# Kernel optimization log

Measured on AMD Instinct MI355X. Metric: run time of the kernel, lower is better.

## Reference

```python
import jax, jax.numpy as jnp
import numpy as np

B, T, E, HID, V, K = 32, 512, 512, 512, 50257, 12
H = HID // 2          # per-direction LSTM hidden
START, STOP = 10, 11  # tag_to_ix['<START>'], tag_to_ix['<STOP>']
NEG = -10000.0


def setup_inputs() -> dict:
    key = jax.random.key(0)
    ks = jax.random.split(key, 16)
    sentence = jax.random.randint(ks[0], (B, T), 0, V)
    embed = jax.random.normal(ks[1], (V, E), jnp.float32) * 0.1
    # torch LSTM weights, gate order (i, f, g, o); biases fused (b_ih + b_hh)
    w_ih_f = jax.random.normal(ks[2], (4 * H, E), jnp.float32) * 0.05
    w_hh_f = jax.random.normal(ks[3], (4 * H, H), jnp.float32) * 0.05
    b_f = jax.random.normal(ks[4], (4 * H,), jnp.float32) * 0.05
    w_ih_b = jax.random.normal(ks[5], (4 * H, E), jnp.float32) * 0.05
    w_hh_b = jax.random.normal(ks[6], (4 * H, H), jnp.float32) * 0.05
    b_b = jax.random.normal(ks[7], (4 * H,), jnp.float32) * 0.05
    # init_hidden(): random initial states, [2 directions, B, H]
    h0 = jax.random.normal(ks[8], (2, B, H), jnp.float32)
    c0 = jax.random.normal(ks[9], (2, B, H), jnp.float32)
    W_out = jax.random.normal(ks[10], (K, HID), jnp.float32) * 0.05
    b_out = jax.random.normal(ks[11], (K,), jnp.float32) * 0.05
    transitions = jax.random.normal(ks[12], (K, K), jnp.float32)
    transitions = transitions.at[START, :].set(NEG).at[:, STOP].set(NEG)
    return dict(sentence=sentence, embed=embed,
                w_ih_f=w_ih_f, w_hh_f=w_hh_f, b_f=b_f,
                w_ih_b=w_ih_b, w_hh_b=w_hh_b, b_b=b_b,
                h0=h0, c0=c0, W_out=W_out, b_out=b_out,
                transitions=transitions)


def _lstm_dir(x, w_ih, w_hh, b, h0, c0, reverse):
    # x: [B, T, E] -> hidden sequence [B, T, H]
    xg = jnp.einsum('bte,ge->btg', x, w_ih) + b  # [B, T, 4H] input pre-activations

    def step(carry, xt):
        h, c = carry
        g = xt + h @ w_hh.T
        i, f, gg, o = jnp.split(g, 4, axis=-1)
        c = jax.nn.sigmoid(f) * c + jax.nn.sigmoid(i) * jnp.tanh(gg)
        h = jax.nn.sigmoid(o) * jnp.tanh(c)
        return (h, c), h

    _, ys = jax.lax.scan(step, (h0, c0), jnp.swapaxes(xg, 0, 1), reverse=reverse)
    return jnp.swapaxes(ys, 0, 1)


def reference(sentence, embed, w_ih_f, w_hh_f, b_f, w_ih_b, w_hh_b, b_b,
              h0, c0, W_out, b_out, transitions):
    # _get_lstm_features
    x = embed[sentence]  # [B, T, E]
    hf = _lstm_dir(x, w_ih_f, w_hh_f, b_f, h0[0], c0[0], False)
    hb = _lstm_dir(x, w_ih_b, w_hh_b, b_b, h0[1], c0[1], True)
    feats = jnp.concatenate([hf, hb], axis=-1) @ W_out.T + b_out  # [B, T, K]

    # _viterbi_decode: fused per-timestep max/argmax recurrence
    init = jnp.full((B, K), NEG, jnp.float32).at[:, START].set(0.0)

    def vstep(fv, feat_t):
        # scores[b, next, prev] = fv[b, prev] + transitions[next, prev]
        scores = fv[:, None, :] + transitions[None, :, :]
        bptr = jnp.argmax(scores, axis=2)            # [B, K]
        fv_new = jnp.max(scores, axis=2) + feat_t     # emit score added after max
        return fv_new, bptr

    fv, bptrs = jax.lax.scan(vstep, init, jnp.swapaxes(feats, 0, 1))  # bptrs [T, B, K]
    terminal = fv + transitions[STOP]                 # [B, K]
    best = jnp.argmax(terminal, axis=1)               # [B]
    # faithful to original: terminal_var[:, best_tag_id] -> [B, B]
    path_score = jnp.take(terminal, best, axis=1)

    def back(tag, bp):
        prev = jnp.take_along_axis(bp, tag[:, None], axis=1)[:, 0]
        return prev, prev

    _, ys = jax.lax.scan(back, best, bptrs, reverse=True)  # ys[t] = tag at position t-1
    # path positions 0..T-1 are (ys[1:], best); ys[0] is START (dropped by [:,1:])
    best_path = jnp.concatenate([ys[1:], best[None, :]], axis=0).T  # [B, T]
    return path_score, best_path
```

## Files before the change

### kernel.cpp

```cpp
#include <hip/hip_runtime.h>
#include <hip/hip_bf16.h>


typedef __attribute__((ext_vector_type(8))) __bf16 bf16x8;
typedef __attribute__((ext_vector_type(8))) unsigned short u16x8;
typedef __attribute__((ext_vector_type(4))) float  f32x4;

#define MFMA16(a, b, c) __builtin_amdgcn_mfma_f32_16x16x32_bf16((a), (b), (c), 0, 0, 0)

__device__ __forceinline__ float sigm(float x) { return 1.0f / (1.0f + __expf(-x)); }
__device__ __forceinline__ float tanh_f(float x) {
  x = fminf(fmaxf(x, -15.0f), 15.0f);
  float e = __expf(2.0f * x);
  return (e - 1.0f) / (e + 1.0f);
}

__device__ __forceinline__ void split8(const float* v, bf16x8& hi, bf16x8& lo) {
#pragma unroll
  for (int j = 0; j < 8; j++) {
    __bf16 h = (__bf16)v[j];
    hi[j] = h;
    lo[j] = (__bf16)(v[j] - (float)h);
  }
}

__global__ __launch_bounds__(256) void xg_gemm(
    const int* __restrict__ sent, const float* __restrict__ embed,
    const float* __restrict__ wih_f, const float* __restrict__ wih_b,
    const float* __restrict__ bias_f, const float* __restrict__ bias_b,
    float* __restrict__ xg)
{
  __shared__ __bf16 Ah[128][40], Al[128][40];
  __shared__ __bf16 Bh[128][40], Bl[128][40];
  __shared__ int toks[128];
  const int tid = threadIdx.x;
  const int m0 = blockIdx.x * 128, n0 = blockIdx.y * 128;
  if (tid < 128) toks[tid] = sent[m0 + tid];
  const int wave = tid >> 6, lane = tid & 63, q = lane >> 4, c = lane & 15;
  const int wy = wave >> 1, wx = wave & 1;
  f32x4 acc[4][4];
  for (int mt = 0; mt < 4; mt++)
    for (int nt = 0; nt < 4; nt++)
      acc[mt][nt] = f32x4{0.0f, 0.0f, 0.0f, 0.0f};
  __syncthreads();

  for (int k0 = 0; k0 < 512; k0 += 32) {
#pragma unroll
    for (int i = 0; i < 2; i++) {
      int ch = tid + (i << 8);
      int r = ch >> 2, kc = ch & 3;
      float tmp[8];
      const float* asrc = embed + (size_t)toks[r] * 512 + k0 + kc * 8;
#pragma unroll
      for (int j = 0; j < 8; j++) tmp[j] = asrc[j];
      bf16x8 hi, lo;
      split8(tmp, hi, lo);
      *(bf16x8*)&Ah[r][kc * 8] = hi;
      *(bf16x8*)&Al[r][kc * 8] = lo;
      int n = n0 + r;
      const float* wsrc = (n < 1024) ? (wih_f + (size_t)n * 512)
                                     : (wih_b + (size_t)(n - 1024) * 512);
#pragma unroll
      for (int j = 0; j < 8; j++) tmp[j] = wsrc[k0 + kc * 8 + j];
      split8(tmp, hi, lo);
      *(bf16x8*)&Bh[r][kc * 8] = hi;
      *(bf16x8*)&Bl[r][kc * 8] = lo;
    }
    __syncthreads();
    bf16x8 ah[4], al[4], bh[4], bl[4];
#pragma unroll
    for (int t4 = 0; t4 < 4; t4++) {
      int ar = wy * 64 + t4 * 16 + c, br = wx * 64 + t4 * 16 + c;
      ah[t4] = *(const bf16x8*)&Ah[ar][q * 8];
      al[t4] = *(const bf16x8*)&Al[ar][q * 8];
      bh[t4] = *(const bf16x8*)&Bh[br][q * 8];
      bl[t4] = *(const bf16x8*)&Bl[br][q * 8];
    }
#pragma unroll
    for (int mt = 0; mt < 4; mt++)
#pragma unroll
      for (int nt = 0; nt < 4; nt++) {
        acc[mt][nt] = MFMA16(ah[mt], bh[nt], acc[mt][nt]);
        acc[mt][nt] = MFMA16(al[mt], bh[nt], acc[mt][nt]);
        acc[mt][nt] = MFMA16(ah[mt], bl[nt], acc[mt][nt]);
      }
    __syncthreads();
  }

#pragma unroll
  for (int nt = 0; nt < 4; nt++) {
    int n = n0 + wx * 64 + nt * 16 + c;
    float bval = (n < 1024) ? bias_f[n] : bias_b[n - 1024];
#pragma unroll
    for (int mt = 0; mt < 4; mt++) {
      int mbase = m0 + wy * 64 + mt * 16 + q * 4;
#pragma unroll
      for (int reg = 0; reg < 4; reg++)
        xg[(size_t)(mbase + reg) * 2048 + n] = acc[mt][nt][reg] + bval;
    }
  }
}

__global__ __launch_bounds__(256, 1) void lstm_rec(
    const float* __restrict__ xg,
    const float* __restrict__ whh_f, const float* __restrict__ whh_b,
    const float* __restrict__ h0, const float* __restrict__ c0,
    float* __restrict__ h_seq,
    unsigned int* __restrict__ hx,
    int* __restrict__ flags)
{
  const int blk = blockIdx.x;
  const int d = blk >> 2, hs = blk & 3;
  const int tid = threadIdx.x;
  const int wave = tid >> 6, lane = tid & 63, q = lane >> 4, c = lane & 15;
  const float* __restrict__ whh = d ? whh_b : whh_f;

  __shared__ __bf16 hfrag[2][16][512];

  bf16x8 wfh[4][8], wfl[4][8];
#pragma unroll
  for (int g = 0; g < 4; g++) {
    int row = g * 256 + hs * 64 + wave * 16 + c;
    const float* wr = whh + (size_t)row * 256;
#pragma unroll
    for (int ks = 0; ks < 8; ks++) {
      float tmp[8];
#pragma unroll
      for (int j = 0; j < 8; j++) tmp[j] = wr[ks * 32 + q * 8 + j];
      split8(tmp, wfh[g][ks], wfl[g][ks]);
    }
  }
  const int ug = hs * 64 + wave * 16 + c;
  float cst[2][4];
#pragma unroll
  for (int mt = 0; mt < 2; mt++)
#pragma unroll
    for (int reg = 0; reg < 4; reg++)
      cst[mt][reg] = c0[d * 8192 + (mt * 16 + q * 4 + reg) * 256 + ug];

  const int sb = tid >> 3;
  const int kc4 = (tid & 7) * 4;

  for (int s = 0; s < 512; s++) {
    const int t_seq = d ? (511 - s) : s;
    const int p = s & 1;

    float xv[2][4][4];
#pragma unroll
    for (int mt = 0; mt < 2; mt++)
#pragma unroll
      for (int reg = 0; reg < 4; reg++) {
        int b = mt * 16 + q * 4 + reg;
        const float* xr = xg + ((size_t)(b * 512 + t_seq) << 11) + (d << 10) + ug;
#pragma unroll
        for (int g = 0; g < 4; g++)
          xv[mt][g][reg] = xr[g << 8];
      }

    if (s > 0) {
      if (tid == 0) {
        while (__hip_atomic_load(&flags[d * 512 + s - 1], __ATOMIC_RELAXED,
                                 __HIP_MEMORY_SCOPE_AGENT) < 4)
          __builtin_amdgcn_s_sleep(1);
      }
      __syncthreads();
    }

    if (s == 0) {
#pragma unroll
      for (int i = 0; i < 4; i++) {
        int kc = kc4 + i;
        float tmp[8];
        const float* src = h0 + d * 8192 + sb * 256 + kc * 8;
#pragma unroll
        for (int j = 0; j < 8; j++) tmp[j] = src[j];
        bf16x8 vhi, vlo;
        split8(tmp, vhi, vlo);
        int fid = ((sb >> 4) << 3) + (kc >> 2);
        int cid = ((kc & 3) << 4) + (sb & 15);
        int pos = cid ^ (fid & 7);
        *(bf16x8*)&hfrag[0][fid][pos * 8] = vhi;
        *(bf16x8*)&hfrag[1][fid][pos * 8] = vlo;
      }
    } else {
      unsigned int vals[4][8];
      const unsigned int* hb = hx + ((size_t)((d * 2 + p) * 32 + sb)) * 256 + kc4 * 8;
#pragma unroll
      for (int i = 0; i < 4; i++)
#pragma unroll
        for (int j = 0; j < 8; j++)
          vals[i][j] = __hip_atomic_load(hb + i * 8 + j, __ATOMIC_RELAXED,
                                         __HIP_MEMORY_SCOPE_AGENT);
#pragma unroll
      for (int i = 0; i < 4; i++) {
        int kc = kc4 + i;
        u16x8 vhi, vlo;
#pragma unroll
        for (int j = 0; j < 8; j++) {
          vhi[j] = (unsigned short)(vals[i][j] >> 16);
          vlo[j] = (unsigned short)(vals[i][j] & 0xffffu);
        }
        int fid = ((sb >> 4) << 3) + (kc >> 2);
        int cid = ((kc & 3) << 4) + (sb & 15);
        int pos = cid ^ (fid & 7);
        *(u16x8*)&hfrag[0][fid][pos * 8] = vhi;
        *(u16x8*)&hfrag[1][fid][pos * 8] = vlo;
      }
    }

    f32x4 acc[2][4];
#pragma unroll
    for (int mt = 0; mt < 2; mt++)
#pragma unroll
      for (int g = 0; g < 4; g++)
#pragma unroll
        for (int reg = 0; reg < 4; reg++)
          acc[mt][g][reg] = xv[mt][g][reg];

    __syncthreads();

#pragma unroll
    for (int ks = 0; ks < 8; ks++) {
      int pos = (lane ^ ks) * 8;
      bf16x8 ahi0 = *(const bf16x8*)&hfrag[0][ks][pos];
      bf16x8 ahi1 = *(const bf16x8*)&hfrag[0][8 + ks][pos];
      bf16x8 alo0 = *(const bf16x8*)&hfrag[1][ks][pos];
      bf16x8 alo1 = *(const bf16x8*)&hfrag[1][8 + ks][pos];
#pragma unroll
      for (int g = 0; g < 4; g++) {
        acc[0][g] = MFMA16(ahi0, wfh[g][ks], acc[0][g]);
        acc[1][g] = MFMA16(ahi1, wfh[g][ks], acc[1][g]);
        acc[0][g] = MFMA16(alo0, wfh[g][ks], acc[0][g]);
        acc[1][g] = MFMA16(alo1, wfh[g][ks], acc[1][g]);
        acc[0][g] = MFMA16(ahi0, wfl[g][ks], acc[0][g]);
        acc[1][g] = MFMA16(ahi1, wfl[g][ks], acc[1][g]);
      }
    }

    const int pn = (s + 1) & 1;
#pragma unroll
    for (int mt = 0; mt < 2; mt++)
#pragma unroll
      for (int reg = 0; reg < 4; reg++) {
        int b = mt * 16 + q * 4 + reg;
        float iv = sigm(acc[mt][0][reg]);
        float fg = sigm(acc[mt][1][reg]);
        float gv = tanh_f(acc[mt][2][reg]);
        float ov = sigm(acc[mt][3][reg]);
        float cn = fg * cst[mt][reg] + iv * gv;
        cst[mt][reg] = cn;
        float hn = ov * tanh_f(cn);
        h_seq[((size_t)(b * 512 + t_seq) << 9) + (d << 8) + ug] = hn;
        __bf16 hhi = (__bf16)hn;
        __bf16 hlo = (__bf16)(hn - (float)hhi);
        unsigned int pack =
            ((unsigned int)__builtin_bit_cast(unsigned short, hhi) << 16) |
            (unsigned int)__builtin_bit_cast(unsigned short, hlo);
        __hip_atomic_store(&hx[((size_t)((d * 2 + pn) * 32 + b)) * 256 + ug], pack,
                           __ATOMIC_RELAXED, __HIP_MEMORY_SCOPE_AGENT);
      }

    __syncthreads();
    if (tid == 0)
      __hip_atomic_fetch_add(&flags[d * 512 + s], 1, __ATOMIC_RELAXED,
                             __HIP_MEMORY_SCOPE_AGENT);
  }
}

__global__ __launch_bounds__(256) void feats_k(
    const float* __restrict__ h_seq, const float* __restrict__ W_out,
    const float* __restrict__ b_out, float* __restrict__ feats)
{
  int m = blockIdx.x * 4 + (threadIdx.x >> 6);
  int lane = threadIdx.x & 63;
  const float4* hp = (const float4*)(h_seq + (size_t)m * 512 + lane * 8);
  float4 a = hp[0], b2 = hp[1];
  float h[8] = {a.x, a.y, a.z, a.w, b2.x, b2.y, b2.z, b2.w};
#pragma unroll
  for (int k = 0; k < 12; k++) {
    const float4* wp = (const float4*)(W_out + k * 512 + lane * 8);
    float4 w0 = wp[0], w1 = wp[1];
    float w[8] = {w0.x, w0.y, w0.z, w0.w, w1.x, w1.y, w1.z, w1.w};
    float p = 0.0f;
#pragma unroll
    for (int j = 0; j < 8; j++) p += h[j] * w[j];
#pragma unroll
    for (int off = 32; off > 0; off >>= 1) p += __shfl_xor(p, off);
    if (lane == 0) feats[(size_t)m * 12 + k] = p + b_out[k];
  }
}

__global__ __launch_bounds__(64) void viterbi_k(
    const float* __restrict__ feats, const float* __restrict__ trans,
    float* __restrict__ terminal, int* __restrict__ best,
    float* __restrict__ out_path)
{
  const int b = blockIdx.x;
  const int lane = threadIdx.x;
  __shared__ unsigned char bp[512][12];
  float trow[12];
#pragma unroll
  for (int pv = 0; pv < 12; pv++)
    trow[pv] = (lane < 12) ? trans[lane * 12 + pv] : -10000.0f;
  float fv = (lane == 10) ? 0.0f : -10000.0f;
  for (int t = 0; t < 512; t++) {
    float bestv = -3.4e38f;
    int arg = 0;
#pragma unroll
    for (int pv = 0; pv < 12; pv++) {
      float sc = __shfl(fv, pv) + trow[pv];
      if (sc > bestv) { bestv = sc; arg = pv; }
    }
    float ft = (lane < 12) ? feats[(size_t)(b * 512 + t) * 12 + lane] : 0.0f;
    if (lane < 12) {
      bp[t][lane] = (unsigned char)arg;
      fv = bestv + ft;
    }
  }
  float term = fv + ((lane < 12) ? trans[11 * 12 + lane] : 0.0f);
  if (lane < 12) terminal[b * 12 + lane] = term;
  float v = (lane < 12) ? term : -3.4e38f;
  int idx = lane;
#pragma unroll
  for (int off = 8; off > 0; off >>= 1) {
    float ov = __shfl_down(v, off);
    int oi = __shfl_down(idx, off);
    if (ov > v || (ov == v && oi < idx)) { v = ov; idx = oi; }
  }
  int bidx = __shfl(idx, 0);
  __syncthreads();
  if (lane == 0) {
    best[b] = bidx;
    int tag = bidx;
    out_path[b * 512 + 511] = (float)bidx;
    for (int t = 511; t >= 1; t--) {
      tag = bp[t][tag];
      out_path[b * 512 + t - 1] = (float)tag;
    }
  }
}

__global__ __launch_bounds__(256) void pscore_k(
    const float* __restrict__ terminal, const int* __restrict__ best,
    float* __restrict__ out)
{
  int idx = blockIdx.x * 256 + threadIdx.x;
  if (idx < 1024) {
    int i = idx >> 5, j = idx & 31;
    out[idx] = terminal[i * 12 + best[j]];
  }
}

extern "C" void kernel_launch(void* const* d_in, const int* in_sizes, int n_in,
                              void* d_out, int out_size, void* d_ws, size_t ws_size,
                              hipStream_t stream)
{
  const int*   sent  = (const int*)d_in[0];
  const float* embed = (const float*)d_in[1];
  const float* wih_f = (const float*)d_in[2];
  const float* whh_f = (const float*)d_in[3];
  const float* b_f   = (const float*)d_in[4];
  const float* wih_b = (const float*)d_in[5];
  const float* whh_b = (const float*)d_in[6];
  const float* b_b   = (const float*)d_in[7];
  const float* h0    = (const float*)d_in[8];
  const float* c0    = (const float*)d_in[9];
  const float* W_out = (const float*)d_in[10];
  const float* b_out = (const float*)d_in[11];
  const float* trans = (const float*)d_in[12];

  char* ws = (char*)d_ws;
  float*        xg    = (float*)(ws);
  float*        h_seq = (float*)(ws + 134217728);
  float*        feats = (float*)(ws + 167772160);
  unsigned int* hx    = (unsigned int*)(ws + 168558592);
  int*          flags = (int*)(ws + 168689664);
  float*        term  = (float*)(ws + 168693760);
  int*          best  = (int*)(ws + 168695296);

  float* outp = (float*)d_out;

  hipMemsetAsync(flags, 0, 2 * 512 * sizeof(int), stream);
  xg_gemm<<<dim3(128, 16), 256, 0, stream>>>(sent, embed, wih_f, wih_b, b_f, b_b, xg);
  lstm_rec<<<8, 256, 0, stream>>>(xg, whh_f, whh_b, h0, c0, h_seq, hx, flags);
  feats_k<<<4096, 256, 0, stream>>>(h_seq, W_out, b_out, feats);
  viterbi_k<<<32, 64, 0, stream>>>(feats, trans, term, best, outp + 1024);
  pscore_k<<<4, 256, 0, stream>>>(term, best, outp);
}
```

Before: 4.594 ms.

## Replace per-step flag barrier with step-tagged hidden-state words in LSTM recurrence

The cross-block handshake in the recurrent LSTM kernel no longer uses a separate flag counter. Each hidden value is now stored as a 64-bit word that carries the step number in its upper half. Readers spin directly on the data until every word they need shows the expected tag. This removes the end-of-step barrier, the flag atomic and the separate flag poll from the serial 512-step critical path. To keep the removed barrier safe, the LDS hidden fragment is double-buffered by step parity. In exchange, the exchanged hidden buffer doubles in width, each reader polls many words instead of one flag, and the buffer now aliases the feats region of the workspace.

```diff
diff --git a/kernel.cpp b/kernel.cpp
--- a/kernel.cpp
+++ b/kernel.cpp
@@ -106,8 +106,7 @@
     const float* __restrict__ whh_f, const float* __restrict__ whh_b,
     const float* __restrict__ h0, const float* __restrict__ c0,
     float* __restrict__ h_seq,
-    unsigned int* __restrict__ hx,
-    int* __restrict__ flags)
+    unsigned long long* __restrict__ hx)
 {
   const int blk = blockIdx.x;
   const int d = blk >> 2, hs = blk & 3;
@@ -115,7 +114,7 @@
   const int wave = tid >> 6, lane = tid & 63, q = lane >> 4, c = lane & 15;
   const float* __restrict__ whh = d ? whh_b : whh_f;
 
-  __shared__ __bf16 hfrag[2][16][512];
+  __shared__ __bf16 hfrag[2][2][16][512];
 
   bf16x8 wfh[4][8], wfl[4][8];
 #pragma unroll
@@ -156,15 +155,6 @@
         for (int g = 0; g < 4; g++)
           xv[mt][g][reg] = xr[g << 8];
       }
-
-    if (s > 0) {
-      if (tid == 0) {
-        while (__hip_atomic_load(&flags[d * 512 + s - 1], __ATOMIC_RELAXED,
-                                 __HIP_MEMORY_SCOPE_AGENT) < 4)
-          __builtin_amdgcn_s_sleep(1);
-      }
-      __syncthreads();
-    }
 
     if (s == 0) {
 #pragma unroll
@@ -179,32 +169,52 @@
         int fid = ((sb >> 4) << 3) + (kc >> 2);
         int cid = ((kc & 3) << 4) + (sb & 15);
         int pos = cid ^ (fid & 7);
-        *(bf16x8*)&hfrag[0][fid][pos * 8] = vhi;
-        *(bf16x8*)&hfrag[1][fid][pos * 8] = vlo;
+        *(bf16x8*)&hfrag[0][0][fid][pos * 8] = vhi;
+        *(bf16x8*)&hfrag[0][1][fid][pos * 8] = vlo;
       }
     } else {
-      unsigned int vals[4][8];
-      const unsigned int* hb = hx + ((size_t)((d * 2 + p) * 32 + sb)) * 256 + kc4 * 8;
+      const unsigned long long want = (unsigned long long)s;
+      unsigned long long v[4][8];
+      const unsigned long long* hb =
+          hx + ((size_t)((d * 2 + p) * 32 + sb)) * 256 + kc4 * 8;
 #pragma unroll
       for (int i = 0; i < 4; i++)
 #pragma unroll
         for (int j = 0; j < 8; j++)
-          vals[i][j] = __hip_atomic_load(hb + i * 8 + j, __ATOMIC_RELAXED,
-                                         __HIP_MEMORY_SCOPE_AGENT);
+          v[i][j] = __hip_atomic_load(hb + i * 8 + j, __ATOMIC_RELAXED,
+                                      __HIP_MEMORY_SCOPE_AGENT);
+      while (true) {
+        bool ok = true;
+#pragma unroll
+        for (int i = 0; i < 4; i++)
+#pragma unroll
+          for (int j = 0; j < 8; j++)
+            if ((v[i][j] >> 32) != want) ok = false;
+        if (ok) break;
+        __builtin_amdgcn_s_sleep(1);
+#pragma unroll
+        for (int i = 0; i < 4; i++)
+#pragma unroll
+          for (int j = 0; j < 8; j++)
+            if ((v[i][j] >> 32) != want)
+              v[i][j] = __hip_atomic_load(hb + i * 8 + j, __ATOMIC_RELAXED,
+                                          __HIP_MEMORY_SCOPE_AGENT);
+      }
 #pragma unroll
       for (int i = 0; i < 4; i++) {
         int kc = kc4 + i;
         u16x8 vhi, vlo;
 #pragma unroll
         for (int j = 0; j < 8; j++) {
-          vhi[j] = (unsigned short)(vals[i][j] >> 16);
-          vlo[j] = (unsigned short)(vals[i][j] & 0xffffu);
+          unsigned int pack = (unsigned int)v[i][j];
+          vhi[j] = (unsigned short)(pack >> 16);
+          vlo[j] = (unsigned short)(pack & 0xffffu);
         }
         int fid = ((sb >> 4) << 3) + (kc >> 2);
         int cid = ((kc & 3) << 4) + (sb & 15);
         int pos = cid ^ (fid & 7);
-        *(u16x8*)&hfrag[0][fid][pos * 8] = vhi;
-        *(u16x8*)&hfrag[1][fid][pos * 8] = vlo;
+        *(u16x8*)&hfrag[p][0][fid][pos * 8] = vhi;
+        *(u16x8*)&hfrag[p][1][fid][pos * 8] = vlo;
       }
     }
 
@@ -222,10 +232,10 @@
 #pragma unroll
     for (int ks = 0; ks < 8; ks++) {
       int pos = (lane ^ ks) * 8;
-      bf16x8 ahi0 = *(const bf16x8*)&hfrag[0][ks][pos];
-      bf16x8 ahi1 = *(const bf16x8*)&hfrag[0][8 + ks][pos];
-      bf16x8 alo0 = *(const bf16x8*)&hfrag[1][ks][pos];
-      bf16x8 alo1 = *(const bf16x8*)&hfrag[1][8 + ks][pos];
+      bf16x8 ahi0 = *(const bf16x8*)&hfrag[p][0][ks][pos];
+      bf16x8 ahi1 = *(const bf16x8*)&hfrag[p][0][8 + ks][pos];
+      bf16x8 alo0 = *(const bf16x8*)&hfrag[p][1][ks][pos];
+      bf16x8 alo1 = *(const bf16x8*)&hfrag[p][1][8 + ks][pos];
 #pragma unroll
       for (int g = 0; g < 4; g++) {
         acc[0][g] = MFMA16(ahi0, wfh[g][ks], acc[0][g]);
@@ -238,6 +248,7 @@
     }
 
     const int pn = (s + 1) & 1;
+    const unsigned long long tag = ((unsigned long long)(s + 1)) << 32;
 #pragma unroll
     for (int mt = 0; mt < 2; mt++)
 #pragma unroll
@@ -256,14 +267,10 @@
         unsigned int pack =
             ((unsigned int)__builtin_bit_cast(unsigned short, hhi) << 16) |
             (unsigned int)__builtin_bit_cast(unsigned short, hlo);
-        __hip_atomic_store(&hx[((size_t)((d * 2 + pn) * 32 + b)) * 256 + ug], pack,
+        __hip_atomic_store(&hx[((size_t)((d * 2 + pn) * 32 + b)) * 256 + ug],
+                           tag | (unsigned long long)pack,
                            __ATOMIC_RELAXED, __HIP_MEMORY_SCOPE_AGENT);
       }
-
-    __syncthreads();
-    if (tid == 0)
-      __hip_atomic_fetch_add(&flags[d * 512 + s], 1, __ATOMIC_RELAXED,
-                             __HIP_MEMORY_SCOPE_AGENT);
   }
 }
 
@@ -370,19 +377,18 @@
   const float* trans = (const float*)d_in[12];
 
   char* ws = (char*)d_ws;
-  float*        xg    = (float*)(ws);
-  float*        h_seq = (float*)(ws + 134217728);
-  float*        feats = (float*)(ws + 167772160);
-  unsigned int* hx    = (unsigned int*)(ws + 168558592);
-  int*          flags = (int*)(ws + 168689664);
-  float*        term  = (float*)(ws + 168693760);
-  int*          best  = (int*)(ws + 168695296);
+  float*              xg    = (float*)(ws);
+  float*              h_seq = (float*)(ws + 134217728);
+  float*              feats = (float*)(ws + 167772160);
+  unsigned long long* hx    = (unsigned long long*)(ws + 167772160);
+  float*              term  = (float*)(ws + 168558592);
+  int*                best  = (int*)(ws + 168560128);
 
   float* outp = (float*)d_out;
 
-  hipMemsetAsync(flags, 0, 2 * 512 * sizeof(int), stream);
+  hipMemsetAsync(hx, 0, 2 * 2 * 32 * 256 * sizeof(unsigned long long), stream);
   xg_gemm<<<dim3(128, 16), 256, 0, stream>>>(sent, embed, wih_f, wih_b, b_f, b_b, xg);
-  lstm_rec<<<8, 256, 0, stream>>>(xg, whh_f, whh_b, h0, c0, h_seq, hx, flags);
+  lstm_rec<<<8, 256, 0, stream>>>(xg, whh_f, whh_b, h0, c0, h_seq, hx);
   feats_k<<<4096, 256, 0, stream>>>(h_seq, W_out, b_out, feats);
   viterbi_k<<<32, 64, 0, stream>>>(feats, trans, term, best, outp + 1024);
   pscore_k<<<4, 256, 0, stream>>>(term, best, outp);
```

New measurement: 5.089 ms. +10.8%, slower.

## Use per-wave flag signaling and double-buffered LDS in LSTM recurrence

Applied to the files above, without the earlier changes.

Drops the block-wide barrier and single-thread spin in the persistent LSTM recurrence. Each wave now polls the step flag itself (waiting for 16 wave arrivals) and signals with its own lane-0 atomic once its hx stores drain. The hidden-state LDS buffer is double-buffered by step parity, which removes the trailing __syncthreads. The hx exchange uses 64-bit atomic loads, and the h_seq store plus the next step's xg prefetch are moved off the critical path after the signal. The cost is more atomic traffic on the flag counters and more registers for the prefetched inputs, and it relies on vmcnt(0) ordering for correctness.

```diff
diff --git a/kernel.cpp b/kernel.cpp
--- a/kernel.cpp
+++ b/kernel.cpp
@@ -115,7 +115,7 @@
   const int wave = tid >> 6, lane = tid & 63, q = lane >> 4, c = lane & 15;
   const float* __restrict__ whh = d ? whh_b : whh_f;
 
-  __shared__ __bf16 hfrag[2][16][512];
+  __shared__ __bf16 hfrag[2][2][16][512];
 
   bf16x8 wfh[4][8], wfl[4][8];
 #pragma unroll
@@ -141,30 +141,25 @@
   const int sb = tid >> 3;
   const int kc4 = (tid & 7) * 4;
 
+  auto load_xv = [&](float (&xv)[2][4][4], int tt) {
+#pragma unroll
+    for (int mt = 0; mt < 2; mt++)
+#pragma unroll
+      for (int reg = 0; reg < 4; reg++) {
+        int b = mt * 16 + q * 4 + reg;
+        const float* xr = xg + ((size_t)(b * 512 + tt) << 11) + (d << 10) + ug;
+#pragma unroll
+        for (int g = 0; g < 4; g++)
+          xv[mt][g][reg] = xr[g << 8];
+      }
+  };
+
+  float xv_cur[2][4][4];
+  load_xv(xv_cur, d ? 511 : 0);
+
   for (int s = 0; s < 512; s++) {
     const int t_seq = d ? (511 - s) : s;
     const int p = s & 1;
-
-    float xv[2][4][4];
-#pragma unroll
-    for (int mt = 0; mt < 2; mt++)
-#pragma unroll
-      for (int reg = 0; reg < 4; reg++) {
-        int b = mt * 16 + q * 4 + reg;
-        const float* xr = xg + ((size_t)(b * 512 + t_seq) << 11) + (d << 10) + ug;
-#pragma unroll
-        for (int g = 0; g < 4; g++)
-          xv[mt][g][reg] = xr[g << 8];
-      }
-
-    if (s > 0) {
-      if (tid == 0) {
-        while (__hip_atomic_load(&flags[d * 512 + s - 1], __ATOMIC_RELAXED,
-                                 __HIP_MEMORY_SCOPE_AGENT) < 4)
-          __builtin_amdgcn_s_sleep(1);
-      }
-      __syncthreads();
-    }
 
     if (s == 0) {
 #pragma unroll
@@ -179,32 +174,38 @@
         int fid = ((sb >> 4) << 3) + (kc >> 2);
         int cid = ((kc & 3) << 4) + (sb & 15);
         int pos = cid ^ (fid & 7);
-        *(bf16x8*)&hfrag[0][fid][pos * 8] = vhi;
-        *(bf16x8*)&hfrag[1][fid][pos * 8] = vlo;
+        *(bf16x8*)&hfrag[0][0][fid][pos * 8] = vhi;
+        *(bf16x8*)&hfrag[0][1][fid][pos * 8] = vlo;
       }
     } else {
-      unsigned int vals[4][8];
-      const unsigned int* hb = hx + ((size_t)((d * 2 + p) * 32 + sb)) * 256 + kc4 * 8;
-#pragma unroll
-      for (int i = 0; i < 4; i++)
-#pragma unroll
-        for (int j = 0; j < 8; j++)
-          vals[i][j] = __hip_atomic_load(hb + i * 8 + j, __ATOMIC_RELAXED,
-                                         __HIP_MEMORY_SCOPE_AGENT);
+      while (__hip_atomic_load(&flags[d * 512 + s - 1], __ATOMIC_RELAXED,
+                               __HIP_MEMORY_SCOPE_AGENT) < 16)
+        __builtin_amdgcn_s_sleep(1);
+
+      const unsigned long long* hb64 = (const unsigned long long*)
+          (hx + ((size_t)((d * 2 + p) * 32 + sb)) * 256 + kc4 * 8);
+      unsigned long long v64[16];
+#pragma unroll
+      for (int i = 0; i < 16; i++)
+        v64[i] = __hip_atomic_load(hb64 + i, __ATOMIC_RELAXED,
+                                   __HIP_MEMORY_SCOPE_AGENT);
 #pragma unroll
       for (int i = 0; i < 4; i++) {
         int kc = kc4 + i;
         u16x8 vhi, vlo;
 #pragma unroll
         for (int j = 0; j < 8; j++) {
-          vhi[j] = (unsigned short)(vals[i][j] >> 16);
-          vlo[j] = (unsigned short)(vals[i][j] & 0xffffu);
+          unsigned long long dv = v64[i * 4 + (j >> 1)];
+          unsigned int w32 = (j & 1) ? (unsigned int)(dv >> 32)
+                                     : (unsigned int)dv;
+          vhi[j] = (unsigned short)(w32 >> 16);
+          vlo[j] = (unsigned short)(w32 & 0xffffu);
         }
         int fid = ((sb >> 4) << 3) + (kc >> 2);
         int cid = ((kc & 3) << 4) + (sb & 15);
         int pos = cid ^ (fid & 7);
-        *(u16x8*)&hfrag[0][fid][pos * 8] = vhi;
-        *(u16x8*)&hfrag[1][fid][pos * 8] = vlo;
+        *(u16x8*)&hfrag[p][0][fid][pos * 8] = vhi;
+        *(u16x8*)&hfrag[p][1][fid][pos * 8] = vlo;
       }
     }
 
@@ -215,17 +216,17 @@
       for (int g = 0; g < 4; g++)
 #pragma unroll
         for (int reg = 0; reg < 4; reg++)
-          acc[mt][g][reg] = xv[mt][g][reg];
+          acc[mt][g][reg] = xv_cur[mt][g][reg];
 
     __syncthreads();
 
 #pragma unroll
     for (int ks = 0; ks < 8; ks++) {
       int pos = (lane ^ ks) * 8;
-      bf16x8 ahi0 = *(const bf16x8*)&hfrag[0][ks][pos];
-      bf16x8 ahi1 = *(const bf16x8*)&hfrag[0][8 + ks][pos];
-      bf16x8 alo0 = *(const bf16x8*)&hfrag[1][ks][pos];
-      bf16x8 alo1 = *(const bf16x8*)&hfrag[1][8 + ks][pos];
+      bf16x8 ahi0 = *(const bf16x8*)&hfrag[p][0][ks][pos];
+      bf16x8 ahi1 = *(const bf16x8*)&hfrag[p][0][8 + ks][pos];
+      bf16x8 alo0 = *(const bf16x8*)&hfrag[p][1][ks][pos];
+      bf16x8 alo1 = *(const bf16x8*)&hfrag[p][1][8 + ks][pos];
 #pragma unroll
       for (int g = 0; g < 4; g++) {
         acc[0][g] = MFMA16(ahi0, wfh[g][ks], acc[0][g]);
@@ -238,6 +239,7 @@
     }
 
     const int pn = (s + 1) & 1;
+    float hv[2][4];
 #pragma unroll
     for (int mt = 0; mt < 2; mt++)
 #pragma unroll
@@ -250,7 +252,7 @@
         float cn = fg * cst[mt][reg] + iv * gv;
         cst[mt][reg] = cn;
         float hn = ov * tanh_f(cn);
-        h_seq[((size_t)(b * 512 + t_seq) << 9) + (d << 8) + ug] = hn;
+        hv[mt][reg] = hn;
         __bf16 hhi = (__bf16)hn;
         __bf16 hlo = (__bf16)(hn - (float)hhi);
         unsigned int pack =
@@ -260,10 +262,30 @@
                            __ATOMIC_RELAXED, __HIP_MEMORY_SCOPE_AGENT);
       }
 
-    __syncthreads();
-    if (tid == 0)
+    asm volatile("s_waitcnt vmcnt(0)" ::: "memory");
+    if (lane == 0)
       __hip_atomic_fetch_add(&flags[d * 512 + s], 1, __ATOMIC_RELAXED,
                              __HIP_MEMORY_SCOPE_AGENT);
+
+#pragma unroll
+    for (int mt = 0; mt < 2; mt++)
+#pragma unroll
+      for (int reg = 0; reg < 4; reg++) {
+        int b = mt * 16 + q * 4 + reg;
+        h_seq[((size_t)(b * 512 + t_seq) << 9) + (d << 8) + ug] = hv[mt][reg];
+      }
+
+    if (s < 511) {
+      float xv_nxt[2][4][4];
+      load_xv(xv_nxt, d ? (511 - (s + 1)) : (s + 1));
+#pragma unroll
+      for (int mt = 0; mt < 2; mt++)
+#pragma unroll
+        for (int g = 0; g < 4; g++)
+#pragma unroll
+          for (int reg = 0; reg < 4; reg++)
+            xv_cur[mt][g][reg] = xv_nxt[mt][g][reg];
+    }
   }
 }
 
```

New measurement: 4.002 ms. 1.15x faster.

## Replace block-barrier flag counting with per-wave flags and prefetch next-step inputs

Applied to the files above, without the earlier changes.

The recurrent LSTM kernel now has each wave publish its own per-step flag slot, and all lanes of every wave poll the 16 producer flags with a wave-wide vote. This replaces the single-thread spin, the block barrier and the atomic counter increment. The xg input for the next step is prefetched into alternating register buffers, and the shared h fragment buffer is double-buffered, which drops one __syncthreads per step. The hi/lo unpacking uses 64-bit loads and byte-permute instructions, and the h_seq store is moved after the flag publish. In exchange, the flags array grows 16x, register pressure rises, and correctness now rests on the explicit vmcnt wait ordering the hx stores before the flag store.

```diff
diff --git a/kernel.cpp b/kernel.cpp
--- a/kernel.cpp
+++ b/kernel.cpp
@@ -3,8 +3,8 @@
 
 
 typedef __attribute__((ext_vector_type(8))) __bf16 bf16x8;
-typedef __attribute__((ext_vector_type(8))) unsigned short u16x8;
 typedef __attribute__((ext_vector_type(4))) float  f32x4;
+typedef __attribute__((ext_vector_type(4))) unsigned int u32x4;
 
 #define MFMA16(a, b, c) __builtin_amdgcn_mfma_f32_16x16x32_bf16((a), (b), (c), 0, 0, 0)
 
@@ -115,7 +115,7 @@
   const int wave = tid >> 6, lane = tid & 63, q = lane >> 4, c = lane & 15;
   const float* __restrict__ whh = d ? whh_b : whh_f;
 
-  __shared__ __bf16 hfrag[2][16][512];
+  __shared__ __bf16 hfrag[2][2][16][512];
 
   bf16x8 wfh[4][8], wfl[4][8];
 #pragma unroll
@@ -141,130 +141,175 @@
   const int sb = tid >> 3;
   const int kc4 = (tid & 7) * 4;
 
-  for (int s = 0; s < 512; s++) {
-    const int t_seq = d ? (511 - s) : s;
-    const int p = s & 1;
-
-    float xv[2][4][4];
-#pragma unroll
-    for (int mt = 0; mt < 2; mt++)
-#pragma unroll
-      for (int reg = 0; reg < 4; reg++) {
-        int b = mt * 16 + q * 4 + reg;
-        const float* xr = xg + ((size_t)(b * 512 + t_seq) << 11) + (d << 10) + ug;
-#pragma unroll
-        for (int g = 0; g < 4; g++)
-          xv[mt][g][reg] = xr[g << 8];
-      }
-
-    if (s > 0) {
-      if (tid == 0) {
-        while (__hip_atomic_load(&flags[d * 512 + s - 1], __ATOMIC_RELAXED,
-                                 __HIP_MEMORY_SCOPE_AGENT) < 4)
-          __builtin_amdgcn_s_sleep(1);
-      }
-      __syncthreads();
-    }
-
-    if (s == 0) {
-#pragma unroll
-      for (int i = 0; i < 4; i++) {
-        int kc = kc4 + i;
-        float tmp[8];
-        const float* src = h0 + d * 8192 + sb * 256 + kc * 8;
-#pragma unroll
-        for (int j = 0; j < 8; j++) tmp[j] = src[j];
-        bf16x8 vhi, vlo;
-        split8(tmp, vhi, vlo);
-        int fid = ((sb >> 4) << 3) + (kc >> 2);
-        int cid = ((kc & 3) << 4) + (sb & 15);
-        int pos = cid ^ (fid & 7);
-        *(bf16x8*)&hfrag[0][fid][pos * 8] = vhi;
-        *(bf16x8*)&hfrag[1][fid][pos * 8] = vlo;
-      }
-    } else {
-      unsigned int vals[4][8];
-      const unsigned int* hb = hx + ((size_t)((d * 2 + p) * 32 + sb)) * 256 + kc4 * 8;
-#pragma unroll
-      for (int i = 0; i < 4; i++)
-#pragma unroll
-        for (int j = 0; j < 8; j++)
-          vals[i][j] = __hip_atomic_load(hb + i * 8 + j, __ATOMIC_RELAXED,
-                                         __HIP_MEMORY_SCOPE_AGENT);
-#pragma unroll
-      for (int i = 0; i < 4; i++) {
-        int kc = kc4 + i;
-        u16x8 vhi, vlo;
-#pragma unroll
-        for (int j = 0; j < 8; j++) {
-          vhi[j] = (unsigned short)(vals[i][j] >> 16);
-          vlo[j] = (unsigned short)(vals[i][j] & 0xffffu);
-        }
-        int fid = ((sb >> 4) << 3) + (kc >> 2);
-        int cid = ((kc & 3) << 4) + (sb & 15);
-        int pos = cid ^ (fid & 7);
-        *(u16x8*)&hfrag[0][fid][pos * 8] = vhi;
-        *(u16x8*)&hfrag[1][fid][pos * 8] = vlo;
-      }
-    }
-
-    f32x4 acc[2][4];
-#pragma unroll
-    for (int mt = 0; mt < 2; mt++)
+  int fid_c[4], pos_c[4];
+#pragma unroll
+  for (int i = 0; i < 4; i++) {
+    int kc = kc4 + i;
+    fid_c[i] = ((sb >> 4) << 3) + (kc >> 2);
+    pos_c[i] = ((((kc & 3) << 4) + (sb & 15)) ^ (fid_c[i] & 7));
+  }
+
+  const unsigned long long* hb64p[2];
+  hb64p[0] = (const unsigned long long*)(hx + ((size_t)((d * 2 + 0) * 32 + sb)) * 256 + kc4 * 8);
+  hb64p[1] = (const unsigned long long*)(hx + ((size_t)((d * 2 + 1) * 32 + sb)) * 256 + kc4 * 8);
+  const int hwbase0 = (d * 2 + 0) * 32 * 256 + ug;
+  const int hwbase1 = (d * 2 + 1) * 32 * 256 + ug;
+  int bof[2][4];
+#pragma unroll
+  for (int mt = 0; mt < 2; mt++)
+#pragma unroll
+    for (int reg = 0; reg < 4; reg++)
+      bof[mt][reg] = (mt * 16 + q * 4 + reg) * 256;
+
+  int fro = (d * 512) * 16 + (lane & 15);
+  int fwo = (d * 512) * 16 + hs * 4 + wave;
+
+  const int t0 = d ? 511 : 0;
+  const int tdelt = d ? -2048 : 2048;
+  const int sdelt = d ? -512 : 512;
+
+  int xgo[2][4], hso[2][4];
+#pragma unroll
+  for (int mt = 0; mt < 2; mt++)
+#pragma unroll
+    for (int reg = 0; reg < 4; reg++) {
+      int b = mt * 16 + q * 4 + reg;
+      xgo[mt][reg] = (b * 512 + t0) * 2048 + (d << 10) + ug;
+      hso[mt][reg] = (b * 512 + t0) * 512 + (d << 8) + ug;
+    }
+
+  float xvA[2][4][4], xvB[2][4][4];
+#pragma unroll
+  for (int mt = 0; mt < 2; mt++)
+#pragma unroll
+    for (int reg = 0; reg < 4; reg++)
 #pragma unroll
       for (int g = 0; g < 4; g++)
-#pragma unroll
-        for (int reg = 0; reg < 4; reg++)
-          acc[mt][g][reg] = xv[mt][g][reg];
-
-    __syncthreads();
-
-#pragma unroll
-    for (int ks = 0; ks < 8; ks++) {
-      int pos = (lane ^ ks) * 8;
-      bf16x8 ahi0 = *(const bf16x8*)&hfrag[0][ks][pos];
-      bf16x8 ahi1 = *(const bf16x8*)&hfrag[0][8 + ks][pos];
-      bf16x8 alo0 = *(const bf16x8*)&hfrag[1][ks][pos];
-      bf16x8 alo1 = *(const bf16x8*)&hfrag[1][8 + ks][pos];
-#pragma unroll
-      for (int g = 0; g < 4; g++) {
-        acc[0][g] = MFMA16(ahi0, wfh[g][ks], acc[0][g]);
-        acc[1][g] = MFMA16(ahi1, wfh[g][ks], acc[1][g]);
-        acc[0][g] = MFMA16(alo0, wfh[g][ks], acc[0][g]);
-        acc[1][g] = MFMA16(alo1, wfh[g][ks], acc[1][g]);
-        acc[0][g] = MFMA16(ahi0, wfl[g][ks], acc[0][g]);
-        acc[1][g] = MFMA16(ahi1, wfl[g][ks], acc[1][g]);
-      }
-    }
-
-    const int pn = (s + 1) & 1;
-#pragma unroll
-    for (int mt = 0; mt < 2; mt++)
-#pragma unroll
-      for (int reg = 0; reg < 4; reg++) {
-        int b = mt * 16 + q * 4 + reg;
-        float iv = sigm(acc[mt][0][reg]);
-        float fg = sigm(acc[mt][1][reg]);
-        float gv = tanh_f(acc[mt][2][reg]);
-        float ov = sigm(acc[mt][3][reg]);
-        float cn = fg * cst[mt][reg] + iv * gv;
-        cst[mt][reg] = cn;
-        float hn = ov * tanh_f(cn);
-        h_seq[((size_t)(b * 512 + t_seq) << 9) + (d << 8) + ug] = hn;
-        __bf16 hhi = (__bf16)hn;
-        __bf16 hlo = (__bf16)(hn - (float)hhi);
-        unsigned int pack =
-            ((unsigned int)__builtin_bit_cast(unsigned short, hhi) << 16) |
-            (unsigned int)__builtin_bit_cast(unsigned short, hlo);
-        __hip_atomic_store(&hx[((size_t)((d * 2 + pn) * 32 + b)) * 256 + ug], pack,
-                           __ATOMIC_RELAXED, __HIP_MEMORY_SCOPE_AGENT);
-      }
-
-    __syncthreads();
-    if (tid == 0)
-      __hip_atomic_fetch_add(&flags[d * 512 + s], 1, __ATOMIC_RELAXED,
-                             __HIP_MEMORY_SCOPE_AGENT);
-  }
+        xvA[mt][g][reg] = xg[xgo[mt][reg] + (g << 8)];
+
+#define LSTM_STEP(S_, P_, XC_, XN_)                                           \
+  {                                                                           \
+    if ((S_) == 0) {                                                          \
+      _Pragma("unroll")                                                       \
+      for (int i = 0; i < 4; i++) {                                           \
+        int kc = kc4 + i;                                                     \
+        float tmp[8];                                                         \
+        const float* src = h0 + d * 8192 + sb * 256 + kc * 8;                 \
+        _Pragma("unroll")                                                     \
+        for (int j = 0; j < 8; j++) tmp[j] = src[j];                          \
+        bf16x8 vhi, vlo;                                                      \
+        split8(tmp, vhi, vlo);                                                \
+        *(bf16x8*)&hfrag[0][0][fid_c[i]][pos_c[i] * 8] = vhi;                 \
+        *(bf16x8*)&hfrag[0][1][fid_c[i]][pos_c[i] * 8] = vlo;                 \
+      }                                                                       \
+    } else {                                                                  \
+      int fv = __hip_atomic_load(flags + fro, __ATOMIC_RELAXED,               \
+                                 __HIP_MEMORY_SCOPE_AGENT);                   \
+      while (!__all(fv == (S_))) {                                            \
+        __builtin_amdgcn_s_sleep(1);                                          \
+        fv = __hip_atomic_load(flags + fro, __ATOMIC_RELAXED,                 \
+                               __HIP_MEMORY_SCOPE_AGENT);                     \
+      }                                                                       \
+      fro += 16;                                                              \
+      unsigned long long v64[16];                                             \
+      _Pragma("unroll")                                                       \
+      for (int i = 0; i < 16; i++)                                            \
+        v64[i] = __hip_atomic_load(hb64p[P_] + i, __ATOMIC_RELAXED,           \
+                                   __HIP_MEMORY_SCOPE_AGENT);                 \
+      _Pragma("unroll")                                                       \
+      for (int i = 0; i < 4; i++) {                                           \
+        u32x4 vh, vl;                                                         \
+        _Pragma("unroll")                                                     \
+        for (int k = 0; k < 4; k++) {                                         \
+          unsigned int lo32 = (unsigned int)v64[i * 4 + k];                   \
+          unsigned int hi32 = (unsigned int)(v64[i * 4 + k] >> 32);           \
+          vh[k] = __builtin_amdgcn_perm(hi32, lo32, 0x07060302u);             \
+          vl[k] = __builtin_amdgcn_perm(hi32, lo32, 0x05040100u);             \
+        }                                                                     \
+        *(u32x4*)&hfrag[P_][0][fid_c[i]][pos_c[i] * 8] = vh;                  \
+        *(u32x4*)&hfrag[P_][1][fid_c[i]][pos_c[i] * 8] = vl;                  \
+      }                                                                       \
+    }                                                                         \
+    f32x4 acc[2][4];                                                          \
+    _Pragma("unroll")                                                         \
+    for (int mt = 0; mt < 2; mt++)                                            \
+      _Pragma("unroll")                                                       \
+      for (int g = 0; g < 4; g++)                                             \
+        _Pragma("unroll")                                                     \
+        for (int reg = 0; reg < 4; reg++)                                     \
+          acc[mt][g][reg] = XC_[mt][g][reg];                                  \
+    __syncthreads();                                                          \
+    _Pragma("unroll")                                                         \
+    for (int ks = 0; ks < 8; ks++) {                                          \
+      int pos = (lane ^ ks) * 8;                                              \
+      bf16x8 ahi0 = *(const bf16x8*)&hfrag[P_][0][ks][pos];                   \
+      bf16x8 ahi1 = *(const bf16x8*)&hfrag[P_][0][8 + ks][pos];               \
+      bf16x8 alo0 = *(const bf16x8*)&hfrag[P_][1][ks][pos];                   \
+      bf16x8 alo1 = *(const bf16x8*)&hfrag[P_][1][8 + ks][pos];               \
+      _Pragma("unroll")                                                       \
+      for (int g = 0; g < 4; g++) {                                           \
+        acc[0][g] = MFMA16(ahi0, wfh[g][ks], acc[0][g]);                      \
+        acc[1][g] = MFMA16(ahi1, wfh[g][ks], acc[1][g]);                      \
+        acc[0][g] = MFMA16(alo0, wfh[g][ks], acc[0][g]);                      \
+        acc[1][g] = MFMA16(alo1, wfh[g][ks], acc[1][g]);                      \
+        acc[0][g] = MFMA16(ahi0, wfl[g][ks], acc[0][g]);                      \
+        acc[1][g] = MFMA16(ahi1, wfl[g][ks], acc[1][g]);                      \
+      }                                                                       \
+    }                                                                         \
+    float hv[2][4];                                                           \
+    _Pragma("unroll")                                                         \
+    for (int mt = 0; mt < 2; mt++)                                            \
+      _Pragma("unroll")                                                       \
+      for (int reg = 0; reg < 4; reg++) {                                     \
+        float iv = sigm(acc[mt][0][reg]);                                     \
+        float fg = sigm(acc[mt][1][reg]);                                     \
+        float gv = tanh_f(acc[mt][2][reg]);                                   \
+        float ov = sigm(acc[mt][3][reg]);                                     \
+        float cn = fg * cst[mt][reg] + iv * gv;                               \
+        cst[mt][reg] = cn;                                                    \
+        float hn = ov * tanh_f(cn);                                           \
+        hv[mt][reg] = hn;                                                     \
+        __bf16 hhi = (__bf16)hn;                                              \
+        __bf16 hlo = (__bf16)(hn - (float)hhi);                               \
+        unsigned int pack =                                                   \
+            ((unsigned int)__builtin_bit_cast(unsigned short, hhi) << 16) |   \
+            (unsigned int)__builtin_bit_cast(unsigned short, hlo);            \
+        __hip_atomic_store(hx + ((P_) ? hwbase0 : hwbase1) + bof[mt][reg],    \
+                           pack, __ATOMIC_RELAXED, __HIP_MEMORY_SCOPE_AGENT); \
+      }                                                                       \
+    asm volatile("s_waitcnt vmcnt(0)" ::: "memory");                          \
+    if (lane == 0)                                                            \
+      __hip_atomic_store(flags + fwo, (S_) + 1, __ATOMIC_RELAXED,             \
+                         __HIP_MEMORY_SCOPE_AGENT);                           \
+    fwo += 16;                                                                \
+    _Pragma("unroll")                                                         \
+    for (int mt = 0; mt < 2; mt++)                                            \
+      _Pragma("unroll")                                                       \
+      for (int reg = 0; reg < 4; reg++)                                       \
+        h_seq[hso[mt][reg]] = hv[mt][reg];                                    \
+    if ((S_) < 511) {                                                         \
+      _Pragma("unroll")                                                       \
+      for (int mt = 0; mt < 2; mt++)                                          \
+        _Pragma("unroll")                                                     \
+        for (int reg = 0; reg < 4; reg++) {                                   \
+          xgo[mt][reg] += tdelt;                                              \
+          hso[mt][reg] += sdelt;                                              \
+        }                                                                     \
+      _Pragma("unroll")                                                       \
+      for (int mt = 0; mt < 2; mt++)                                          \
+        _Pragma("unroll")                                                     \
+        for (int reg = 0; reg < 4; reg++)                                     \
+          _Pragma("unroll")                                                   \
+          for (int g = 0; g < 4; g++)                                         \
+            XN_[mt][g][reg] = xg[xgo[mt][reg] + (g << 8)];                    \
+    }                                                                         \
+  }
+
+  for (int s = 0; s < 512; s += 2) {
+    LSTM_STEP(s,     0, xvA, xvB);
+    LSTM_STEP(s + 1, 1, xvB, xvA);
+  }
+#undef LSTM_STEP
 }
 
 __global__ __launch_bounds__(256) void feats_k(
@@ -375,12 +420,12 @@
   float*        feats = (float*)(ws + 167772160);
   unsigned int* hx    = (unsigned int*)(ws + 168558592);
   int*          flags = (int*)(ws + 168689664);
-  float*        term  = (float*)(ws + 168693760);
-  int*          best  = (int*)(ws + 168695296);
+  float*        term  = (float*)(ws + 168755200);
+  int*          best  = (int*)(ws + 168756736);
 
   float* outp = (float*)d_out;
 
-  hipMemsetAsync(flags, 0, 2 * 512 * sizeof(int), stream);
+  hipMemsetAsync(flags, 0, 2 * 512 * 16 * sizeof(int), stream);
   xg_gemm<<<dim3(128, 16), 256, 0, stream>>>(sent, embed, wih_f, wih_b, b_f, b_b, xg);
   lstm_rec<<<8, 256, 0, stream>>>(xg, whh_f, whh_b, h0, c0, h_seq, hx, flags);
   feats_k<<<4096, 256, 0, stream>>>(h_seq, W_out, b_out, feats);
```

Result: faster. 3.856 ms (median of 2 runs) (-16.1%).
